# Kernel tuning notes

Measured on AMD Instinct MI355X. Metric: run time of the kernel, lower is better.

## Reference

```python
import jax, jax.numpy as jnp
import numpy as np

MARGIN = 0.2  # TripletMarginLoss margin and TripletMarginMiner margin


def setup_inputs() -> dict:
    key = jax.random.key(0)
    k1, k2 = jax.random.split(key)
    embeddings = jax.random.normal(k1, (384, 256), dtype=jnp.float32)
    labels = jax.random.randint(k2, (384,), 0, 32)
    return {"embeddings": embeddings, "labels": labels}


def _pairwise_l2(e):
    # Euclidean distance matrix with sqrt-safe gradient at zero.
    sq = jnp.sum(e * e, axis=1)
    d2 = jnp.maximum(sq[:, None] + sq[None, :] - 2.0 * (e @ e.T), 0.0)
    pos = d2 > 0.0
    return jnp.sqrt(jnp.where(pos, d2, 1.0)) * pos


def reference(embeddings, labels):
    # pytorch-metric-learning LpDistance defaults: normalize_embeddings=True, p=2
    e = embeddings / jnp.maximum(
        jnp.linalg.norm(embeddings, axis=1, keepdims=True), 1e-12
    )
    D = _pairwise_l2(e)  # [B, B]
    n = D.shape[0]

    same = labels[:, None] == labels[None, :]
    eye = jnp.eye(n, dtype=bool)
    pos_mask = same & ~eye   # valid (anchor, positive) pairs
    neg_mask = ~same         # valid (anchor, negative) pairs

    ap = D[:, :, None]       # dist(anchor, positive), broadcast over negative
    an = D[:, None, :]       # dist(anchor, negative), broadcast over positive
    tm = an - ap             # miner's triplet_margin (is_inverted=False)

    valid = pos_mask[:, :, None] & neg_mask[:, None, :]     # [B, B, B]
    # semihard miner: 0 < an - ap <= margin
    semihard = valid & (tm > 0.0) & (tm <= MARGIN)

    # TripletMarginLoss per-triplet loss: relu(ap - an + margin) = relu(margin - tm)
    losses = jnp.where(semihard, jnp.maximum(MARGIN - tm, 0.0), 0.0)

    # AvgNonZeroReducer: mean over strictly-positive losses (0 if none)
    nz = jnp.sum(losses > 0.0)
    total = jnp.sum(losses)
    return jnp.where(nz > 0, total / jnp.maximum(nz, 1).astype(total.dtype), 0.0)
```

## Files before the change

### kernel.cpp

```cpp
#include <hip/hip_runtime.h>

#define N        384
#define DIM      256
#define D4       (DIM / 4)
#define CHUNK_K4 8
#define NCHUNK   4
#define MARGIN_F 0.2f
#define NANCH    2
#define NBLK     (N / NANCH)
#define NTHR     (2 * N)
#define NWAVE    (NTHR / 64)
#define MAXPOS   64
#define LROW     (CHUNK_K4 + 1)


__global__ __launch_bounds__(NTHR) void triplet_kernel(
    const float4* __restrict__ emb4, const int* __restrict__ labels,
    float* __restrict__ accum_sum, unsigned int* __restrict__ accum_cnt,
    unsigned int* __restrict__ done_cnt, float* __restrict__ out)
{
    const int i0   = blockIdx.x * NANCH;
    const int tid  = threadIdx.x;
    const int wave = tid >> 6, lane = tid & 63;
    const int kgrp = (tid >= N) ? 1 : 0;
    const int col  = tid - kgrp * N;

    __shared__ float4 ebuf[2][N][LROW];
    __shared__ float  pacc[3][N];
    __shared__ float  Drow[NANCH][N];
    __shared__ float  invA[NANCH], sqA[NANCH];
    __shared__ int    lab[N];
    __shared__ int    posList[NANCH][MAXPOS];
    __shared__ int    posCnt[NANCH];
    __shared__ float        sredS[NWAVE];
    __shared__ unsigned int sredC[NWAVE];

    if (tid < N) lab[tid] = labels[tid];
    if (tid < NANCH) posCnt[tid] = 0;

    float vv = 0.0f, rd0 = 0.0f, rd1 = 0.0f;
    const int kbase = kgrp * (NCHUNK * CHUNK_K4);

    for (int c = 0; c < NCHUNK; ++c) {
        const int kk0 = kbase + c * CHUNK_K4;
        #pragma unroll
        for (int i = 0; i < 8; ++i) {
            const int s   = i * N + col;
            const int row = s >> 3, j = s & 7;
            ebuf[kgrp][row][j] = emb4[row * D4 + kk0 + j];
        }
        __syncthreads();
        #pragma unroll
        for (int j = 0; j < CHUNK_K4; ++j) {
            const float4 v  = ebuf[kgrp][col][j];
            const float4 a0 = ebuf[kgrp][i0][j];
            const float4 a1 = ebuf[kgrp][i0 + 1][j];
            vv  += v.x*v.x  + v.y*v.y  + v.z*v.z  + v.w*v.w;
            rd0 += v.x*a0.x + v.y*a0.y + v.z*a0.z + v.w*a0.w;
            rd1 += v.x*a1.x + v.y*a1.y + v.z*a1.z + v.w*a1.w;
        }
        __syncthreads();
    }

    if (kgrp == 1) { pacc[0][col] = vv; pacc[1][col] = rd0; pacc[2][col] = rd1; }
    __syncthreads();

    float inv_j = 0.0f, sq_j = 0.0f;
    if (kgrp == 0) {
        vv  += pacc[0][col];
        rd0 += pacc[1][col];
        rd1 += pacc[2][col];
        inv_j = 1.0f / fmaxf(sqrtf(vv), 1e-12f);
        sq_j  = vv * inv_j * inv_j;
        if (col == i0)     { invA[0] = inv_j; sqA[0] = sq_j; }
        if (col == i0 + 1) { invA[1] = inv_j; sqA[1] = sq_j; }
    } else {
        const int lj = lab[col];
        #pragma unroll
        for (int a = 0; a < NANCH; ++a) {
            const int ia = i0 + a;
            if (lj == lab[ia] && col != ia)
                posList[a][atomicAdd(&posCnt[a], 1)] = col;
        }
    }
    __syncthreads();

    if (kgrp == 0) {
        float d2 = fmaxf(sqA[0] + sq_j - 2.0f * (rd0 * (invA[0] * inv_j)), 0.0f);
        Drow[0][col] = (d2 > 0.0f) ? sqrtf(d2) : 0.0f;
        d2       = fmaxf(sqA[1] + sq_j - 2.0f * (rd1 * (invA[1] * inv_j)), 0.0f);
        Drow[1][col] = (d2 > 0.0f) ? sqrtf(d2) : 0.0f;
    }
    __syncthreads();

    float        lsum = 0.0f;
    unsigned int lcnt = 0u;
    {
        const int a  = kgrp;
        const int li = lab[i0 + a];
        if (lab[col] != li) {
            const float dk = Drow[a][col];
            const int   np = posCnt[a];
            for (int p = 0; p < np; ++p) {
                const float tm = dk - Drow[a][posList[a][p]];
                if (tm > 0.0f && tm <= MARGIN_F) {
                    const float l = MARGIN_F - tm;
                    lsum += l;
                    if (l > 0.0f) lcnt++;
                }
            }
        }
    }

    #pragma unroll
    for (int off = 32; off > 0; off >>= 1) {
        lsum += __shfl_down(lsum, off, 64);
        lcnt += __shfl_down(lcnt, off, 64);
    }
    if (lane == 0) { sredS[wave] = lsum; sredC[wave] = lcnt; }
    __syncthreads();

    if (tid == 0) {
        float        S = 0.0f;
        unsigned int C = 0u;
        #pragma unroll
        for (int w = 0; w < NWAVE; ++w) { S += sredS[w]; C += sredC[w]; }
        if (S != 0.0f || C != 0u) {
            atomicAdd(accum_sum, S);
            atomicAdd(accum_cnt, C);
        }
        __threadfence();
        const unsigned int prev = atomicAdd(done_cnt, 1);
        if (prev == NBLK - 1) {
            const float        Sall = atomicAdd(accum_sum, 0.0f);
            const unsigned int Call = atomicAdd(accum_cnt, 0u);
            out[0] = (Call > 0u) ? (Sall / (float)Call) : 0.0f;
        }
    }
}

extern "C" void kernel_launch(void* const* d_in, const int* in_sizes, int n_in,
                              void* d_out, int out_size, void* d_ws, size_t ws_size,
                              hipStream_t stream) {
    const float4* emb4   = (const float4*)d_in[0];
    const int*    labels = (const int*)d_in[1];
    float*        out    = (float*)d_out;

    float*        accum_sum = (float*)d_ws;
    unsigned int* accum_cnt = (unsigned int*)accum_sum + 1;
    unsigned int* done_cnt  = (unsigned int*)accum_sum + 2;

    hipMemsetAsync(d_ws, 0, 16, stream);
    triplet_kernel<<<NBLK, NTHR, 0, stream>>>(emb4, labels,
                                              accum_sum, accum_cnt, done_cnt, out);
}
```

Measured before the change: 73.10 us.

## Prefetch embedding chunks into registers with swizzled double-buffered LDS and slotted atomics

Each thread now loads the next embedding chunk from global memory into registers while the current chunk is being computed. Shared memory is double-buffered, so one barrier per chunk is enough instead of two. An XOR swizzle on the float4 column replaces the padded row to avoid bank conflicts, and the two k-groups split each chunk's columns rather than separate halves of the dimension. The global sum and count atomics are spread over 8 padded slots, and wave 0 of the last block reduces them. The cost is more registers per thread and a larger workspace memset.

```diff
diff --git a/kernel.cpp b/kernel.cpp
--- a/kernel.cpp
+++ b/kernel.cpp
@@ -3,20 +3,20 @@
 #define N        384
 #define DIM      256
 #define D4       (DIM / 4)
-#define CHUNK_K4 8
-#define NCHUNK   4
+#define CK4      8
+#define NCH      8
 #define MARGIN_F 0.2f
 #define NANCH    2
 #define NBLK     (N / NANCH)
 #define NTHR     (2 * N)
 #define NWAVE    (NTHR / 64)
 #define MAXPOS   64
-#define LROW     (CHUNK_K4 + 1)
+#define NSLOT    8
 
 
 __global__ __launch_bounds__(NTHR) void triplet_kernel(
     const float4* __restrict__ emb4, const int* __restrict__ labels,
-    float* __restrict__ accum_sum, unsigned int* __restrict__ accum_cnt,
+    float* __restrict__ sumSlots, unsigned int* __restrict__ cntSlots,
     unsigned int* __restrict__ done_cnt, float* __restrict__ out)
 {
     const int i0   = blockIdx.x * NANCH;
@@ -25,7 +25,11 @@
     const int kgrp = (tid >= N) ? 1 : 0;
     const int col  = tid - kgrp * N;
 
-    __shared__ float4 ebuf[2][N][LROW];
+    const int rbase = tid >> 3;
+    const int js    = tid & 7;
+    const int swz   = js ^ (rbase & 7);
+
+    __shared__ float4 ebuf[2][N][CK4];
     __shared__ float  pacc[3][N];
     __shared__ float  Drow[NANCH][N];
     __shared__ float  invA[NANCH], sqA[NANCH];
@@ -34,32 +38,42 @@
     __shared__ int    posCnt[NANCH];
     __shared__ float        sredS[NWAVE];
     __shared__ unsigned int sredC[NWAVE];
+    __shared__ int    isLastSh;
+
+    float4 rr[4];
+    #pragma unroll
+    for (int i = 0; i < 4; ++i)
+        rr[i] = emb4[i * (96 * D4) + rbase * D4 + js];
 
     if (tid < N) lab[tid] = labels[tid];
     if (tid < NANCH) posCnt[tid] = 0;
 
     float vv = 0.0f, rd0 = 0.0f, rd1 = 0.0f;
-    const int kbase = kgrp * (NCHUNK * CHUNK_K4);
+    const int j0 = kgrp * 4;
+    const int sa0 = i0 & 7, sa1 = (i0 + 1) & 7;
 
-    for (int c = 0; c < NCHUNK; ++c) {
-        const int kk0 = kbase + c * CHUNK_K4;
+    #pragma unroll
+    for (int c = 0; c < NCH; ++c) {
+        const int cur = c & 1;
         #pragma unroll
-        for (int i = 0; i < 8; ++i) {
-            const int s   = i * N + col;
-            const int row = s >> 3, j = s & 7;
-            ebuf[kgrp][row][j] = emb4[row * D4 + kk0 + j];
+        for (int i = 0; i < 4; ++i)
+            ebuf[cur][i * 96 + rbase][swz] = rr[i];
+        if (c + 1 < NCH) {
+            #pragma unroll
+            for (int i = 0; i < 4; ++i)
+                rr[i] = emb4[i * (96 * D4) + rbase * D4 + (c + 1) * CK4 + js];
         }
         __syncthreads();
         #pragma unroll
-        for (int j = 0; j < CHUNK_K4; ++j) {
-            const float4 v  = ebuf[kgrp][col][j];
-            const float4 a0 = ebuf[kgrp][i0][j];
-            const float4 a1 = ebuf[kgrp][i0 + 1][j];
+        for (int jj = 0; jj < 4; ++jj) {
+            const int j = j0 + jj;
+            const float4 v  = ebuf[cur][col][j ^ (col & 7)];
+            const float4 a0 = ebuf[cur][i0][j ^ sa0];
+            const float4 a1 = ebuf[cur][i0 + 1][j ^ sa1];
             vv  += v.x*v.x  + v.y*v.y  + v.z*v.z  + v.w*v.w;
             rd0 += v.x*a0.x + v.y*a0.y + v.z*a0.z + v.w*a0.w;
             rd1 += v.x*a1.x + v.y*a1.y + v.z*a1.z + v.w*a1.w;
         }
-        __syncthreads();
     }
 
     if (kgrp == 1) { pacc[0][col] = vv; pacc[1][col] = rd0; pacc[2][col] = rd1; }
@@ -126,16 +140,28 @@
         #pragma unroll
         for (int w = 0; w < NWAVE; ++w) { S += sredS[w]; C += sredC[w]; }
         if (S != 0.0f || C != 0u) {
-            atomicAdd(accum_sum, S);
-            atomicAdd(accum_cnt, C);
+            atomicAdd(&sumSlots[(blockIdx.x & (NSLOT - 1)) * 16], S);
+            atomicAdd(&cntSlots[(blockIdx.x & (NSLOT - 1)) * 16], C);
         }
         __threadfence();
         const unsigned int prev = atomicAdd(done_cnt, 1);
-        if (prev == NBLK - 1) {
-            const float        Sall = atomicAdd(accum_sum, 0.0f);
-            const unsigned int Call = atomicAdd(accum_cnt, 0u);
-            out[0] = (Call > 0u) ? (Sall / (float)Call) : 0.0f;
+        isLastSh = (prev == NBLK - 1) ? 1 : 0;
+    }
+    __syncthreads();
+
+    if (isLastSh && wave == 0) {
+        float        s = 0.0f;
+        unsigned int c = 0u;
+        if (lane < NSLOT) {
+            s = atomicAdd(&sumSlots[lane * 16], 0.0f);
+            c = atomicAdd(&cntSlots[lane * 16], 0u);
         }
+        #pragma unroll
+        for (int off = 4; off > 0; off >>= 1) {
+            s += __shfl_down(s, off, 64);
+            c += __shfl_down(c, off, 64);
+        }
+        if (lane == 0) out[0] = (c > 0u) ? (s / (float)c) : 0.0f;
     }
 }
 
@@ -146,11 +172,11 @@
     const int*    labels = (const int*)d_in[1];
     float*        out    = (float*)d_out;
 
-    float*        accum_sum = (float*)d_ws;
-    unsigned int* accum_cnt = (unsigned int*)accum_sum + 1;
-    unsigned int* done_cnt  = (unsigned int*)accum_sum + 2;
+    unsigned int* done_cnt = (unsigned int*)d_ws;
+    float*        sumSlots = (float*)((char*)d_ws + 64);
+    unsigned int* cntSlots = (unsigned int*)((char*)d_ws + 576);
 
-    hipMemsetAsync(d_ws, 0, 16, stream);
+    hipMemsetAsync(d_ws, 0, 1088, stream);
     triplet_kernel<<<NBLK, NTHR, 0, stream>>>(emb4, labels,
-                                              accum_sum, accum_cnt, done_cnt, out);
+                                              sumSlots, cntSlots, done_cnt, out);
 }
```

Measured after the change: 93.98 us. 28.6% more time.
